# Kernel optimization log

Measured on AMD Instinct MI355X. Metric: run time of the kernel, lower is better.

Reference implementation:

```python
import jax, jax.numpy as jnp
import numpy as np

N_NODES = 50000
N_EDGES = 800000
D_IN = 96
HID = 96
D_OUT = 64
NUM_LAYERS = 6  # conv1 + (NUM_LAYERS-2) hidden convs + out_conv


def gcn_conv(x, W, b, src, dst, n):
    """PyG GCNConv: add self-loops, symmetric D^-1/2 (A+I) D^-1/2 normalization."""
    h = x @ W  # [n, out_dim]
    loops = jnp.arange(n, dtype=src.dtype)
    s = jnp.concatenate([src, loops])
    d = jnp.concatenate([dst, loops])
    deg = jax.ops.segment_sum(jnp.ones_like(s, dtype=h.dtype), d, num_segments=n)
    dinv = jnp.where(deg > 0, jax.lax.rsqrt(deg), 0.0)
    norm = dinv[s] * dinv[d]                 # [E+n]
    msg = h[s] * norm[:, None]               # gather + scale
    out = jax.ops.segment_sum(msg, d, num_segments=n)  # scatter-add to targets
    return out + b


def setup_inputs() -> dict:
    key = jax.random.key(0)
    ks = jax.random.split(key, 10)
    x = jax.random.normal(ks[0], (N_NODES, D_IN), dtype=jnp.float32)
    edge_index = jax.random.randint(ks[1], (2, N_EDGES), 0, N_NODES, dtype=jnp.int32)
    ricci_curvature = jax.random.normal(ks[2], (N_EDGES,), dtype=jnp.float32)
    n_hidden = NUM_LAYERS - 2
    W1 = jax.random.normal(ks[3], (D_IN, HID), dtype=jnp.float32) * 0.05
    b1 = jnp.zeros((HID,), dtype=jnp.float32)
    Ws = jax.random.normal(ks[4], (n_hidden, HID, HID), dtype=jnp.float32) * 0.05
    bs = jnp.zeros((n_hidden, HID), dtype=jnp.float32)
    Wout = jax.random.normal(ks[5], ((NUM_LAYERS - 1) * HID, D_OUT), dtype=jnp.float32) * 0.05
    bout = jnp.zeros((D_OUT,), dtype=jnp.float32)
    return {
        "x": x, "edge_index": edge_index, "percent": 70,
        "ricci_curvature": ricci_curvature,
        "W1": W1, "b1": b1, "Ws": Ws, "bs": bs, "Wout": Wout, "bout": bout,
    }


def reference(x, edge_index, percent, ricci_curvature, W1, b1, Ws, bs, Wout, bout):
    # Eval path: no sampling / dynamic reweighting, dropout is identity, no BN.
    del percent, ricci_curvature
    n = x.shape[0]
    src, dst = edge_index[0], edge_index[1]
    res = []
    h = jax.nn.relu(gcn_conv(x, W1, b1, src, dst, n))
    res.append(h)
    for i in range(Ws.shape[0]):
        h = jax.nn.relu(gcn_conv(h, Ws[i], bs[i], src, dst, n))
        res.append(h)
    x_cat = jnp.concatenate(res, axis=1)  # JK concatenation: [n, (L-1)*HID]
    out = gcn_conv(x_cat, Wout, bout, src, dst, n)
    return (out,) + tuple(res)
```

## Files before the change

kernel.cpp:

```cpp
#include <hip/hip_runtime.h>


typedef unsigned short ushortT;
typedef __attribute__((ext_vector_type(8))) short bf16x8;
typedef __attribute__((ext_vector_type(4))) float f32x4;

__device__ __forceinline__ ushortT f2b(float f) {
    union { float f; unsigned int u; } v;
    v.f = f;
    unsigned int lsb = (v.u >> 16) & 1u;
    v.u += 0x7fffu + lsb;
    return (ushortT)(v.u >> 16);
}
__device__ __forceinline__ float b2f(ushortT u) {
    union { float f; unsigned int u; } v;
    v.u = ((unsigned int)u) << 16;
    return v.f;
}

__global__ void prep_kernel(const float* __restrict__ W1, const float* __restrict__ Wsl,
                            const float* __restrict__ Wout, ushortT* __restrict__ wt1,
                            ushortT* __restrict__ wts, ushortT* __restrict__ wto,
                            int* __restrict__ degi, int n) {
    const int SQ = 96 * 96;
    const int T1 = 5 * SQ;
    const int T2 = T1 + 480 * 64;
    int i = blockIdx.x * blockDim.x + threadIdx.x;
    if (i < T1) {
        int l = i / SQ, j = i - l * SQ;
        int c = j / 96, k = j - c * 96;
        if (l == 0)
            wt1[j] = f2b(W1[k * 96 + c]);
        else
            wts[(size_t)(l - 1) * SQ + j] = f2b(Wsl[(size_t)(l - 1) * SQ + k * 96 + c]);
    } else if (i < T2) {
        int j = i - T1;
        int c = j / 480, k = j - c * 480;
        wto[j] = f2b(Wout[(size_t)k * 64 + c]);
    } else {
        int j = i - T2;
        if (j < n) degi[j] = 0;
    }
}

__global__ void count_kernel(const int* __restrict__ dst, int* __restrict__ degi, int E) {
    int e = blockIdx.x * blockDim.x + threadIdx.x;
    if (e < E) atomicAdd(&degi[dst[e]], 1);
}

__global__ void scan1(const int* __restrict__ degi, int* __restrict__ row_start,
                      int* __restrict__ partials, int n) {
    __shared__ int tmp[256];
    const int t = threadIdx.x;
    const int i = blockIdx.x * 256 + t;
    int val = (i < n) ? degi[i] : 0;
    tmp[t] = val;
    __syncthreads();
    for (int off = 1; off < 256; off <<= 1) {
        int v = (t >= off) ? tmp[t - off] : 0;
        __syncthreads();
        tmp[t] += v;
        __syncthreads();
    }
    if (i < n) row_start[i] = tmp[t] - val;
    if (t == 255) partials[blockIdx.x] = tmp[255];
}

__global__ void scan2(int* __restrict__ partials, int nb) {
    __shared__ int tmp[256];
    const int t = threadIdx.x;
    int val = (t < nb) ? partials[t] : 0;
    tmp[t] = val;
    __syncthreads();
    for (int off = 1; off < 256; off <<= 1) {
        int v = (t >= off) ? tmp[t - off] : 0;
        __syncthreads();
        tmp[t] += v;
        __syncthreads();
    }
    if (t < nb) partials[t] = tmp[t] - val;
}

__global__ void scan3(const int* __restrict__ degi, int* __restrict__ row_start,
                      const int* __restrict__ partials, float* __restrict__ dinv,
                      int n, int E) {
    const int i = blockIdx.x * 256 + threadIdx.x;
    if (i < n) {
        row_start[i] += partials[blockIdx.x];
        dinv[i] = rsqrtf((float)degi[i] + 1.0f);
    }
    if (i == 0) row_start[n] = E;
}

__global__ void fill_kernel(const int* __restrict__ src, const int* __restrict__ dst,
                            const int* __restrict__ row_start, int* __restrict__ degi,
                            int* __restrict__ col, int E) {
    int e = blockIdx.x * blockDim.x + threadIdx.x;
    if (e < E) {
        int d = dst[e];
        int pos = row_start[d] + atomicSub(&degi[d], 1) - 1;
        col[pos] = src[e];
    }
}

template <typename TIN>
__global__ __launch_bounds__(256) void gemm96_mfma(const TIN* __restrict__ X,
                                                   const ushortT* __restrict__ Wt,
                                                   const float* __restrict__ dinv,
                                                   ushortT* __restrict__ g, int n) {
    __shared__ __attribute__((aligned(16))) ushortT Xl[64][104];
    __shared__ __attribute__((aligned(16))) ushortT Wtl[96][104];
    const int tid = threadIdx.x;
    const int wave = tid >> 6, lane = tid & 63;
    const int quad = lane >> 4, m = lane & 15;
    const int row_base = blockIdx.x * 64;
    for (int i = tid; i < 96 * 24; i += 256) {
        int r = i / 24, c4 = (i % 24) * 4;
        *(ushort4*)&Wtl[r][c4] = *(const ushort4*)&Wt[r * 96 + c4];
    }
    for (int i = tid; i < 64 * 24; i += 256) {
        int r = i / 24, c4 = (i % 24) * 4;
        int grow = min(row_base + r, n - 1);
        if constexpr (sizeof(TIN) == 4) {
            float4 v = *(const float4*)&X[(size_t)grow * 96 + c4];
            ushort4 o = {f2b(v.x), f2b(v.y), f2b(v.z), f2b(v.w)};
            *(ushort4*)&Xl[r][c4] = o;
        } else {
            *(ushort4*)&Xl[r][c4] = *(const ushort4*)&X[(size_t)grow * 96 + c4];
        }
    }
    __syncthreads();
    f32x4 acc[6] = {};
#pragma unroll
    for (int ks = 0; ks < 3; ++ks) {
        bf16x8 a = *(bf16x8*)&Xl[wave * 16 + m][ks * 32 + quad * 8];
#pragma unroll
        for (int ct = 0; ct < 6; ++ct) {
            bf16x8 b = *(bf16x8*)&Wtl[ct * 16 + m][ks * 32 + quad * 8];
            acc[ct] = __builtin_amdgcn_mfma_f32_16x16x32_bf16(a, b, acc[ct], 0, 0, 0);
        }
    }
    float di[4];
    int rows[4];
#pragma unroll
    for (int r = 0; r < 4; ++r) {
        rows[r] = row_base + wave * 16 + quad * 4 + r;
        di[r] = (rows[r] < n) ? dinv[rows[r]] : 0.f;
    }
#pragma unroll
    for (int ct = 0; ct < 6; ++ct) {
        int colx = ct * 16 + m;
#pragma unroll
        for (int r = 0; r < 4; ++r)
            if (rows[r] < n) g[(size_t)rows[r] * 96 + colx] = f2b(acc[ct][r] * di[r]);
    }
}

template <typename TIN>
__global__ __launch_bounds__(256) void gemm_out_mfma(const TIN* __restrict__ hcat,
                                                     const ushortT* __restrict__ Wt,
                                                     const float* __restrict__ dinv,
                                                     ushortT* __restrict__ g, int n) {
    __shared__ __attribute__((aligned(16))) ushortT Xl[64][104];
    __shared__ __attribute__((aligned(16))) ushortT Wtl[64][104];
    const int tid = threadIdx.x;
    const int wave = tid >> 6, lane = tid & 63;
    const int quad = lane >> 4, m = lane & 15;
    const int row_base = blockIdx.x * 64;
    f32x4 acc[4] = {};
    for (int seg = 0; seg < 5; ++seg) {
        const TIN* hl = hcat + (size_t)seg * (size_t)n * 96;
        __syncthreads();
        for (int i = tid; i < 64 * 24; i += 256) {
            int r = i / 24, c4 = (i % 24) * 4;
            *(ushort4*)&Wtl[r][c4] = *(const ushort4*)&Wt[r * 480 + seg * 96 + c4];
        }
        for (int i = tid; i < 64 * 24; i += 256) {
            int r = i / 24, c4 = (i % 24) * 4;
            int grow = min(row_base + r, n - 1);
            if constexpr (sizeof(TIN) == 4) {
                float4 v = *(const float4*)&hl[(size_t)grow * 96 + c4];
                ushort4 o = {f2b(v.x), f2b(v.y), f2b(v.z), f2b(v.w)};
                *(ushort4*)&Xl[r][c4] = o;
            } else {
                *(ushort4*)&Xl[r][c4] = *(const ushort4*)&hl[(size_t)grow * 96 + c4];
            }
        }
        __syncthreads();
#pragma unroll
        for (int ks = 0; ks < 3; ++ks) {
            bf16x8 a = *(bf16x8*)&Xl[wave * 16 + m][ks * 32 + quad * 8];
#pragma unroll
            for (int ct = 0; ct < 4; ++ct) {
                bf16x8 b = *(bf16x8*)&Wtl[ct * 16 + m][ks * 32 + quad * 8];
                acc[ct] = __builtin_amdgcn_mfma_f32_16x16x32_bf16(a, b, acc[ct], 0, 0, 0);
            }
        }
    }
    float di[4];
    int rows[4];
#pragma unroll
    for (int r = 0; r < 4; ++r) {
        rows[r] = row_base + wave * 16 + quad * 4 + r;
        di[r] = (rows[r] < n) ? dinv[rows[r]] : 0.f;
    }
#pragma unroll
    for (int ct = 0; ct < 4; ++ct) {
        int colx = ct * 16 + m;
#pragma unroll
        for (int r = 0; r < 4; ++r)
            if (rows[r] < n) g[(size_t)rows[r] * 64 + colx] = f2b(acc[ct][r] * di[r]);
    }
}

template <int F, bool RELU, bool WRITE_BF16>
__global__ void agg_csr(const int* __restrict__ row_start, const int* __restrict__ col,
                        const ushortT* __restrict__ g, const float* __restrict__ dinv,
                        const float* __restrict__ b, float* __restrict__ out,
                        ushortT* __restrict__ hb, int n) {
    constexpr int NV = F / 4;
    const int lane = threadIdx.x & 63;
    const int half = lane >> 5;
    const int l32 = lane & 31;
    const int v = blockIdx.x * (blockDim.x >> 6) + (threadIdx.x >> 6);
    if (v >= n) return;
    const int e0 = row_start[v];
    const int e1 = row_start[v + 1];
    const bool act = (l32 < NV);
    const size_t fo = (size_t)l32 * 4;
    float a0 = 0.f, a1 = 0.f, a2 = 0.f, a3 = 0.f;
    float s0 = 0.f, s1 = 0.f, s2 = 0.f, s3 = 0.f;
    if (half == 0 && act) {
        ushort4 s = *(const ushort4*)&g[(size_t)v * F + fo];
        a0 = b2f(s.x); a1 = b2f(s.y); a2 = b2f(s.z); a3 = b2f(s.w);
    }
    int e = e0 + half;
    for (; e + 6 < e1; e += 8) {
        int c0 = col[e], c1 = col[e + 2], c2 = col[e + 4], c3 = col[e + 6];
        if (act) {
            ushort4 g0 = *(const ushort4*)&g[(size_t)c0 * F + fo];
            ushort4 g1 = *(const ushort4*)&g[(size_t)c1 * F + fo];
            ushort4 g2 = *(const ushort4*)&g[(size_t)c2 * F + fo];
            ushort4 g3 = *(const ushort4*)&g[(size_t)c3 * F + fo];
            a0 += b2f(g0.x) + b2f(g1.x); s0 += b2f(g2.x) + b2f(g3.x);
            a1 += b2f(g0.y) + b2f(g1.y); s1 += b2f(g2.y) + b2f(g3.y);
            a2 += b2f(g0.z) + b2f(g1.z); s2 += b2f(g2.z) + b2f(g3.z);
            a3 += b2f(g0.w) + b2f(g1.w); s3 += b2f(g2.w) + b2f(g3.w);
        }
    }
    for (; e + 2 < e1; e += 4) {
        int c0 = col[e], c1 = col[e + 2];
        if (act) {
            ushort4 g0 = *(const ushort4*)&g[(size_t)c0 * F + fo];
            ushort4 g1 = *(const ushort4*)&g[(size_t)c1 * F + fo];
            a0 += b2f(g0.x) + b2f(g1.x);
            a1 += b2f(g0.y) + b2f(g1.y);
            a2 += b2f(g0.z) + b2f(g1.z);
            a3 += b2f(g0.w) + b2f(g1.w);
        }
    }
    for (; e < e1; e += 2) {
        int c = col[e];
        if (act) {
            ushort4 g0 = *(const ushort4*)&g[(size_t)c * F + fo];
            a0 += b2f(g0.x); a1 += b2f(g0.y); a2 += b2f(g0.z); a3 += b2f(g0.w);
        }
    }
    a0 += s0; a1 += s1; a2 += s2; a3 += s3;
    a0 += __shfl_xor(a0, 32);
    a1 += __shfl_xor(a1, 32);
    a2 += __shfl_xor(a2, 32);
    a3 += __shfl_xor(a3, 32);
    if (half == 0 && act) {
        const float di = dinv[v];
        const float4 bv = *(const float4*)&b[l32 * 4];
        float4 r;
        r.x = a0 * di + bv.x;
        r.y = a1 * di + bv.y;
        r.z = a2 * di + bv.z;
        r.w = a3 * di + bv.w;
        if (RELU) {
            r.x = fmaxf(r.x, 0.f); r.y = fmaxf(r.y, 0.f);
            r.z = fmaxf(r.z, 0.f); r.w = fmaxf(r.w, 0.f);
        }
        *(float4*)&out[(size_t)v * F + l32 * 4] = r;
        if (WRITE_BF16) {
            ushort4 o = {f2b(r.x), f2b(r.y), f2b(r.z), f2b(r.w)};
            *(ushort4*)&hb[(size_t)v * F + l32 * 4] = o;
        }
    }
}

extern "C" void kernel_launch(void* const* d_in, const int* in_sizes, int n_in,
                              void* d_out, int out_size, void* d_ws, size_t ws_size,
                              hipStream_t stream) {
    const float* x    = (const float*)d_in[0];
    const int*   ei   = (const int*)d_in[1];
    const float* W1   = (const float*)d_in[4];
    const float* b1   = (const float*)d_in[5];
    const float* Wsl  = (const float*)d_in[6];
    const float* bsl  = (const float*)d_in[7];
    const float* Wout = (const float*)d_in[8];
    const float* bout = (const float*)d_in[9];

    const int n = in_sizes[0] / 96;
    const int E = in_sizes[1] / 2;
    const int* src = ei;
    const int* dst = ei + E;

    char* p = (char*)d_ws;
    int*     degi      = (int*)p;              p += (size_t)n * 4;
    int*     row_start = (int*)p;              p += (size_t)(n + 1) * 4;
    int*     partials  = (int*)p;              p += 256 * 4;
    int*     col       = (int*)p;              p += (size_t)E * 4;
    float*   dinv      = (float*)p;            p += (size_t)n * 4;
    ushortT* g         = (ushortT*)p;          p += (size_t)n * 96 * 2;
    ushortT* hball     = (ushortT*)p;
    const size_t wbytes = (size_t)(5 * 9216 + 30720) * 2;
    const size_t fixed  = (size_t)(p - (char*)d_ws);
    const bool   big    = (fixed + (size_t)5 * n * 96 * 2 + wbytes) <= ws_size;
    const size_t hbsz   = big ? (size_t)5 * n * 96 : (size_t)n * 96;
    p += hbsz * 2;
    ushortT* wt1 = (ushortT*)p;
    ushortT* wts = wt1 + 5 * 9216 - 4 * 9216;
    wts = wt1 + 9216;
    ushortT* wto = wts + 4 * 9216;

    float* out  = (float*)d_out;
    float* hseg = out + (size_t)n * 64;

    const int nthr = 256;
    const int gE   = (E + nthr - 1) / nthr;
    const int gAgg = (n + 3) / 4;
    const int gT64 = (n + 63) / 64;
    const int nb   = (n + 255) / 256;

    const int prep_items = 76800 + n;
    prep_kernel<<<(prep_items + 255) / 256, 256, 0, stream>>>(W1, Wsl, Wout, wt1, wts,
                                                              wto, degi, n);

    count_kernel<<<gE, nthr, 0, stream>>>(dst, degi, E);
    scan1<<<nb, 256, 0, stream>>>(degi, row_start, partials, n);
    scan2<<<1, 256, 0, stream>>>(partials, nb);
    scan3<<<nb, 256, 0, stream>>>(degi, row_start, partials, dinv, n, E);
    fill_kernel<<<gE, nthr, 0, stream>>>(src, dst, row_start, degi, col, E);

    ushortT* hb0 = hball;
    gemm96_mfma<float><<<gT64, 256, 0, stream>>>(x, wt1, dinv, g, n);
    agg_csr<96, true, true><<<gAgg, nthr, 0, stream>>>(row_start, col, g, dinv, b1,
                                                       hseg, hb0, n);

    for (int l = 0; l < 4; ++l) {
        float*   hnext = hseg + (size_t)(l + 1) * (size_t)n * 96;
        ushortT* hbin  = big ? (hball + (size_t)l * n * 96) : hball;
        ushortT* hbout = big ? (hball + (size_t)(l + 1) * n * 96) : hball;
        gemm96_mfma<ushortT><<<gT64, 256, 0, stream>>>(hbin, wts + (size_t)l * 9216,
                                                       dinv, g, n);
        agg_csr<96, true, true><<<gAgg, nthr, 0, stream>>>(row_start, col, g, dinv,
                                                           bsl + (size_t)l * 96, hnext,
                                                           hbout, n);
    }

    if (big)
        gemm_out_mfma<ushortT><<<gT64, 256, 0, stream>>>(hball, wto, dinv, g, n);
    else
        gemm_out_mfma<float><<<gT64, 256, 0, stream>>>(hseg, wto, dinv, g, n);
    agg_csr<64, false, false><<<gAgg, nthr, 0, stream>>>(row_start, col, g, dinv, bout,
                                                         out, nullptr, n);
}
```

Before: 523.9 us.

## Split gathered features into 32-wide planes and aggregate several rows per wave

```diff
diff --git a/kernel.cpp b/kernel.cpp
--- a/kernel.cpp
+++ b/kernel.cpp
@@ -114,6 +114,7 @@
     const int wave = tid >> 6, lane = tid & 63;
     const int quad = lane >> 4, m = lane & 15;
     const int row_base = blockIdx.x * 64;
+    const size_t pstride = (size_t)n * 32;
     for (int i = tid; i < 96 * 24; i += 256) {
         int r = i / 24, c4 = (i % 24) * 4;
         *(ushort4*)&Wtl[r][c4] = *(const ushort4*)&Wt[r * 96 + c4];
@@ -149,10 +150,13 @@
     }
 #pragma unroll
     for (int ct = 0; ct < 6; ++ct) {
-        int colx = ct * 16 + m;
+        const int plane = ct >> 1;
+        const int pcol = (ct & 1) * 16 + m;
 #pragma unroll
         for (int r = 0; r < 4; ++r)
-            if (rows[r] < n) g[(size_t)rows[r] * 96 + colx] = f2b(acc[ct][r] * di[r]);
+            if (rows[r] < n)
+                g[(size_t)plane * pstride + (size_t)rows[r] * 32 + pcol] =
+                    f2b(acc[ct][r] * di[r]);
     }
 }
 
@@ -167,6 +171,7 @@
     const int wave = tid >> 6, lane = tid & 63;
     const int quad = lane >> 4, m = lane & 15;
     const int row_base = blockIdx.x * 64;
+    const size_t pstride = (size_t)n * 32;
     f32x4 acc[4] = {};
     for (int seg = 0; seg < 5; ++seg) {
         const TIN* hl = hcat + (size_t)seg * (size_t)n * 96;
@@ -206,88 +211,112 @@
     }
 #pragma unroll
     for (int ct = 0; ct < 4; ++ct) {
-        int colx = ct * 16 + m;
+        const int plane = ct >> 1;
+        const int pcol = (ct & 1) * 16 + m;
 #pragma unroll
         for (int r = 0; r < 4; ++r)
-            if (rows[r] < n) g[(size_t)rows[r] * 64 + colx] = f2b(acc[ct][r] * di[r]);
-    }
-}
-
-template <int F, bool RELU, bool WRITE_BF16>
-__global__ void agg_csr(const int* __restrict__ row_start, const int* __restrict__ col,
-                        const ushortT* __restrict__ g, const float* __restrict__ dinv,
-                        const float* __restrict__ b, float* __restrict__ out,
-                        ushortT* __restrict__ hb, int n) {
-    constexpr int NV = F / 4;
+            if (rows[r] < n)
+                g[(size_t)plane * pstride + (size_t)rows[r] * 32 + pcol] =
+                    f2b(acc[ct][r] * di[r]);
+    }
+}
+
+template <int NPLANES, int HW, bool RELU, bool WRITE_BF16>
+__global__ __launch_bounds__(256, 8) void agg_planes(
+        const int* __restrict__ row_start, const int* __restrict__ col,
+        const ushortT* __restrict__ g, const float* __restrict__ dinv,
+        const float* __restrict__ bias, float* __restrict__ out,
+        ushortT* __restrict__ hb, int n) {
+    constexpr int RPW = 7;
     const int lane = threadIdx.x & 63;
-    const int half = lane >> 5;
-    const int l32 = lane & 31;
-    const int v = blockIdx.x * (blockDim.x >> 6) + (threadIdx.x >> 6);
-    if (v >= n) return;
-    const int e0 = row_start[v];
-    const int e1 = row_start[v + 1];
-    const bool act = (l32 < NV);
-    const size_t fo = (size_t)l32 * 4;
-    float a0 = 0.f, a1 = 0.f, a2 = 0.f, a3 = 0.f;
-    float s0 = 0.f, s1 = 0.f, s2 = 0.f, s3 = 0.f;
-    if (half == 0 && act) {
-        ushort4 s = *(const ushort4*)&g[(size_t)v * F + fo];
-        a0 = b2f(s.x); a1 = b2f(s.y); a2 = b2f(s.z); a3 = b2f(s.w);
-    }
-    int e = e0 + half;
-    for (; e + 6 < e1; e += 8) {
-        int c0 = col[e], c1 = col[e + 2], c2 = col[e + 4], c3 = col[e + 6];
-        if (act) {
-            ushort4 g0 = *(const ushort4*)&g[(size_t)c0 * F + fo];
-            ushort4 g1 = *(const ushort4*)&g[(size_t)c1 * F + fo];
-            ushort4 g2 = *(const ushort4*)&g[(size_t)c2 * F + fo];
-            ushort4 g3 = *(const ushort4*)&g[(size_t)c3 * F + fo];
-            a0 += b2f(g0.x) + b2f(g1.x); s0 += b2f(g2.x) + b2f(g3.x);
-            a1 += b2f(g0.y) + b2f(g1.y); s1 += b2f(g2.y) + b2f(g3.y);
-            a2 += b2f(g0.z) + b2f(g1.z); s2 += b2f(g2.z) + b2f(g3.z);
-            a3 += b2f(g0.w) + b2f(g1.w); s3 += b2f(g2.w) + b2f(g3.w);
-        }
-    }
-    for (; e + 2 < e1; e += 4) {
-        int c0 = col[e], c1 = col[e + 2];
-        if (act) {
-            ushort4 g0 = *(const ushort4*)&g[(size_t)c0 * F + fo];
-            ushort4 g1 = *(const ushort4*)&g[(size_t)c1 * F + fo];
-            a0 += b2f(g0.x) + b2f(g1.x);
-            a1 += b2f(g0.y) + b2f(g1.y);
-            a2 += b2f(g0.z) + b2f(g1.z);
-            a3 += b2f(g0.w) + b2f(g1.w);
-        }
-    }
-    for (; e < e1; e += 2) {
-        int c = col[e];
-        if (act) {
-            ushort4 g0 = *(const ushort4*)&g[(size_t)c * F + fo];
-            a0 += b2f(g0.x); a1 += b2f(g0.y); a2 += b2f(g0.z); a3 += b2f(g0.w);
-        }
-    }
-    a0 += s0; a1 += s1; a2 += s2; a3 += s3;
-    a0 += __shfl_xor(a0, 32);
-    a1 += __shfl_xor(a1, 32);
-    a2 += __shfl_xor(a2, 32);
-    a3 += __shfl_xor(a3, 32);
-    if (half == 0 && act) {
-        const float di = dinv[v];
-        const float4 bv = *(const float4*)&b[l32 * 4];
-        float4 r;
-        r.x = a0 * di + bv.x;
-        r.y = a1 * di + bv.y;
-        r.z = a2 * di + bv.z;
-        r.w = a3 * di + bv.w;
-        if (RELU) {
-            r.x = fmaxf(r.x, 0.f); r.y = fmaxf(r.y, 0.f);
-            r.z = fmaxf(r.z, 0.f); r.w = fmaxf(r.w, 0.f);
-        }
-        *(float4*)&out[(size_t)v * F + l32 * 4] = r;
-        if (WRITE_BF16) {
-            ushort4 o = {f2b(r.x), f2b(r.y), f2b(r.z), f2b(r.w)};
-            *(ushort4*)&hb[(size_t)v * F + l32 * 4] = o;
-        }
+    const int f8 = lane & 7;
+    const int eslot = lane >> 3;
+    const int gw = blockIdx.x * (blockDim.x >> 6) + (threadIdx.x >> 6);
+    const int r0 = gw * RPW;
+    const size_t pstride = (size_t)n * 32;
+
+    int e0a[RPW], dga[RPW], cva[RPW];
+    float dva[RPW];
+#pragma unroll
+    for (int i = 0; i < RPW; ++i) {
+        const int row = r0 + i;
+        e0a[i] = 0; dga[i] = 0; dva[i] = 0.f; cva[i] = 0;
+        if (row < n) {
+            const int e0 = row_start[row];
+            const int e1 = row_start[row + 1];
+            e0a[i] = e0;
+            dga[i] = e1 - e0;
+            dva[i] = dinv[row];
+            if (lane < min(e1 - e0, 64)) cva[i] = col[e0 + lane];
+        }
+    }
+
+#pragma unroll
+    for (int p = 0; p < NPLANES; ++p) {
+        const ushortT* gp = g + (size_t)p * pstride;
+        const float4 bv = *(const float4*)&bias[p * 32 + f8 * 4];
+#pragma unroll
+        for (int i = 0; i < RPW; ++i) {
+            const int row = r0 + i;
+            if (row < n) {
+                const int deg = dga[i];
+                float a0 = 0.f, a1 = 0.f, a2 = 0.f, a3 = 0.f;
+                if (eslot == 0) {
+                    ushort4 s = *(const ushort4*)&gp[(size_t)row * 32 + f8 * 4];
+                    a0 = b2f(s.x); a1 = b2f(s.y); a2 = b2f(s.z); a3 = b2f(s.w);
+                }
+                const int kc = min(deg, 64);
+                const int rounds = (kc + 7) >> 3;
+                for (int r = 0; r < rounds; ++r) {
+                    const int idx = (r << 3) + eslot;
+                    const int c = __shfl(cva[i], idx);
+                    if (idx < kc) {
+                        ushort4 gg = *(const ushort4*)&gp[(size_t)c * 32 + f8 * 4];
+                        a0 += b2f(gg.x); a1 += b2f(gg.y);
+                        a2 += b2f(gg.z); a3 += b2f(gg.w);
+                    }
+                }
+                if (deg > 64) {
+                    for (int done = 64; done < deg; done += 64) {
+                        const int kc2 = min(deg - done, 64);
+                        int cv2 = 0;
+                        if (lane < kc2) cv2 = col[e0a[i] + done + lane];
+                        const int rr = (kc2 + 7) >> 3;
+                        for (int r = 0; r < rr; ++r) {
+                            const int idx = (r << 3) + eslot;
+                            const int c = __shfl(cv2, idx);
+                            if (idx < kc2) {
+                                ushort4 gg = *(const ushort4*)&gp[(size_t)c * 32 + f8 * 4];
+                                a0 += b2f(gg.x); a1 += b2f(gg.y);
+                                a2 += b2f(gg.z); a3 += b2f(gg.w);
+                            }
+                        }
+                    }
+                }
+                a0 += __shfl_xor(a0, 8); a0 += __shfl_xor(a0, 16); a0 += __shfl_xor(a0, 32);
+                a1 += __shfl_xor(a1, 8); a1 += __shfl_xor(a1, 16); a1 += __shfl_xor(a1, 32);
+                a2 += __shfl_xor(a2, 8); a2 += __shfl_xor(a2, 16); a2 += __shfl_xor(a2, 32);
+                a3 += __shfl_xor(a3, 8); a3 += __shfl_xor(a3, 16); a3 += __shfl_xor(a3, 32);
+                if (lane < 8) {
+                    const float di = dva[i];
+                    float4 rv;
+                    rv.x = a0 * di + bv.x;
+                    rv.y = a1 * di + bv.y;
+                    rv.z = a2 * di + bv.z;
+                    rv.w = a3 * di + bv.w;
+                    if (RELU) {
+                        rv.x = fmaxf(rv.x, 0.f); rv.y = fmaxf(rv.y, 0.f);
+                        rv.z = fmaxf(rv.z, 0.f); rv.w = fmaxf(rv.w, 0.f);
+                    }
+                    *(float4*)&out[(size_t)row * HW + p * 32 + lane * 4] = rv;
+                    if (WRITE_BF16) {
+                        ushort4 o = {f2b(rv.x), f2b(rv.y), f2b(rv.z), f2b(rv.w)};
+                        *(ushort4*)&hb[(size_t)row * 96 + p * 32 + lane * 4] = o;
+                    }
+                }
+            }
+        }
+        __syncthreads();
     }
 }
 
@@ -322,18 +351,17 @@
     const size_t hbsz   = big ? (size_t)5 * n * 96 : (size_t)n * 96;
     p += hbsz * 2;
     ushortT* wt1 = (ushortT*)p;
-    ushortT* wts = wt1 + 5 * 9216 - 4 * 9216;
-    wts = wt1 + 9216;
+    ushortT* wts = wt1 + 9216;
     ushortT* wto = wts + 4 * 9216;
 
     float* out  = (float*)d_out;
     float* hseg = out + (size_t)n * 64;
 
-    const int nthr = 256;
-    const int gE   = (E + nthr - 1) / nthr;
-    const int gAgg = (n + 3) / 4;
-    const int gT64 = (n + 63) / 64;
-    const int nb   = (n + 255) / 256;
+    const int nthr  = 256;
+    const int gE    = (E + nthr - 1) / nthr;
+    const int gT64  = (n + 63) / 64;
+    const int nb    = (n + 255) / 256;
+    const int gAggP = (n + 4 * 7 - 1) / (4 * 7);
 
     const int prep_items = 76800 + n;
     prep_kernel<<<(prep_items + 255) / 256, 256, 0, stream>>>(W1, Wsl, Wout, wt1, wts,
@@ -345,10 +373,9 @@
     scan3<<<nb, 256, 0, stream>>>(degi, row_start, partials, dinv, n, E);
     fill_kernel<<<gE, nthr, 0, stream>>>(src, dst, row_start, degi, col, E);
 
-    ushortT* hb0 = hball;
     gemm96_mfma<float><<<gT64, 256, 0, stream>>>(x, wt1, dinv, g, n);
-    agg_csr<96, true, true><<<gAgg, nthr, 0, stream>>>(row_start, col, g, dinv, b1,
-                                                       hseg, hb0, n);
+    agg_planes<3, 96, true, true><<<gAggP, nthr, 0, stream>>>(
+        row_start, col, g, dinv, b1, hseg, hball, n);
 
     for (int l = 0; l < 4; ++l) {
         float*   hnext = hseg + (size_t)(l + 1) * (size_t)n * 96;
@@ -356,15 +383,14 @@
         ushortT* hbout = big ? (hball + (size_t)(l + 1) * n * 96) : hball;
         gemm96_mfma<ushortT><<<gT64, 256, 0, stream>>>(hbin, wts + (size_t)l * 9216,
                                                        dinv, g, n);
-        agg_csr<96, true, true><<<gAgg, nthr, 0, stream>>>(row_start, col, g, dinv,
-                                                           bsl + (size_t)l * 96, hnext,
-                                                           hbout, n);
+        agg_planes<3, 96, true, true><<<gAggP, nthr, 0, stream>>>(
+            row_start, col, g, dinv, bsl + (size_t)l * 96, hnext, hbout, n);
     }
 
     if (big)
         gemm_out_mfma<ushortT><<<gT64, 256, 0, stream>>>(hball, wto, dinv, g, n);
     else
         gemm_out_mfma<float><<<gT64, 256, 0, stream>>>(hseg, wto, dinv, g, n);
-    agg_csr<64, false, false><<<gAgg, nthr, 0, stream>>>(row_start, col, g, dinv, bout,
-                                                         out, nullptr, n);
-}
+    agg_planes<2, 64, false, false><<<gAggP, nthr, 0, stream>>>(
+        row_start, col, g, dinv, bout, out, nullptr, n);
+}
```

Result: slower. 615.0 us (+17.4%).
